# Kernel tuning notes

Hardware: AMD Instinct MI355X
Metric: run time of the kernel (lower is better)

The kernel has to match this reference:

```python
import jax, jax.numpy as jnp
import numpy as np

B, T, C, H, DI = 4, 1024, 1024, 16, 128
TAU = 1.0
LAMBDA_CONF = 0.1
SYS2_THR = 1.0


def _ln(x, w, b):
    mu = x.mean(-1, keepdims=True)
    var = x.var(-1, keepdims=True)
    return (x - mu) * jax.lax.rsqrt(var + 1e-5) * w + b


def setup_inputs() -> dict:
    key = jax.random.key(0)
    ks = jax.random.split(key, 16)
    s = lambda i, shape: jax.random.normal(ks[i], shape, jnp.float32) * 0.02
    return {
        "h": jax.random.normal(ks[0], (B, T, C), jnp.float32),
        "ln_w": jnp.ones((C,), jnp.float32), "ln_b": jnp.zeros((C,), jnp.float32),
        "w_q": s(1, (C, C)), "w_k": s(2, (C, C)), "w_v": s(3, (C, C)),
        "w_o": s(4, (C, C)), "b_o": jnp.zeros((C,), jnp.float32),
        "U": s(5, (C, DI)), "V": s(6, (DI, C)),
        "gamma_w": s(7, (C, 1)), "gamma_b": jnp.zeros((1,), jnp.float32),
        "mass_w": s(8, (C, 1)), "mass_b": jnp.zeros((1,), jnp.float32),
        "eps_w": s(9, (C, 1)), "eps_b": jnp.zeros((1,), jnp.float32),
        "lg_w1": s(10, (C, 4 * C)), "lg_b1": jnp.zeros((4 * C,), jnp.float32),
        "lg_w2": s(11, (4 * C, C)), "lg_b2": jnp.zeros((C,), jnp.float32),
        "mlp_w1": s(12, (C, 4 * C)), "mlp_b1": jnp.zeros((4 * C,), jnp.float32),
        "mlp_w2": s(13, (4 * C, C)), "mlp_b2": jnp.zeros((C,), jnp.float32),
    }


def reference(h, ln_w, ln_b, w_q, w_k, w_v, w_o, b_o, U, V,
              gamma_w, gamma_b, mass_w, mass_b, eps_w, eps_b,
              lg_w1, lg_b1, lg_w2, lg_b2, mlp_w1, mlp_b1, mlp_w2, mlp_b2):
    hd = C // H
    h_norm = _ln(h, ln_w, ln_b)

    # ---- HamiltonianAttention (conservative force field) ----
    q = (h_norm @ w_q).reshape(B, T, H, hd).transpose(0, 2, 1, 3)  # [B,H,T,hd]
    k = (h_norm @ w_k).reshape(B, T, H, hd).transpose(0, 2, 1, 3)
    v = (h_norm @ w_v).reshape(B, T, H, hd).transpose(0, 2, 1, 3)
    scores = jnp.einsum('bhqd,bhkd->bhqk', q, k) / (hd ** 0.5) / TAU
    attn = jax.nn.softmax(scores, axis=-1)
    force = jnp.einsum('bhqk,bhkd->bhqd', attn, v).transpose(0, 2, 1, 3).reshape(B, T, C)
    f_attn = force @ w_o + b_o

    # ---- total force, low-rank projection ----
    f_total = f_attn - LAMBDA_CONF * h_norm
    f_proj = f_total @ U                               # [B,T,DI]

    # ---- FSI (force stability index) ----
    h_mag = jnp.linalg.norm(h_norm, axis=-1)           # [B,T]
    f_mag = jnp.linalg.norm(f_proj, axis=-1)
    fsi = h_mag / (2.0 * f_mag + 1e-6)

    # ---- CognitiveGearbox: per-token mass / timestep ----
    mass = 1.0 + jax.nn.softplus(h @ mass_w + mass_b)  # [B,T,1], mass >= 1
    eps = jax.nn.sigmoid(h @ eps_w + eps_b)            # [B,T,1], eps in (0,1)
    gamma = jax.nn.sigmoid(h_norm @ gamma_w + gamma_b) # [B,T,1] damping gate

    # ---- fused AGI momentum recurrence: m_t = gamma_t*m_{t-1} + (eps_t/mass_t)*f_t ----
    def step(m, inps):
        f_t, g_t, e_t, ms_t = inps                     # [B,DI],[B,1],[B,1],[B,1]
        m = g_t * m + (e_t / ms_t) * f_t
        return m, m

    xs = (f_proj.transpose(1, 0, 2), gamma.transpose(1, 0, 2),
          eps.transpose(1, 0, 2), mass.transpose(1, 0, 2))
    m0 = jnp.zeros((B, DI), h.dtype)
    _, m_seq = jax.lax.scan(step, m0, xs)              # [T,B,DI]
    m_new = m_seq.transpose(1, 0, 2)                   # [B,T,DI]

    # ---- position update + system-2 correction + MLP ----
    velocity = m_new @ V                               # [B,T,C]
    h_new = h + eps * velocity
    hn2 = _ln(h_new, ln_w, ln_b)
    sys2 = jax.nn.gelu(hn2 @ lg_w1 + lg_b1, approximate=False) @ lg_w2 + lg_b2
    gate = jax.nn.sigmoid(mass - SYS2_THR)
    h_final = h_new + gate * sys2
    hn3 = _ln(h_final, ln_w, ln_b)
    h_final = h_final + (jax.nn.gelu(hn3 @ mlp_w1 + mlp_b1, approximate=False) @ mlp_w2 + mlp_b2)
    return (h_final, m_new, fsi)
```

## Files before the change

### kernel.cpp

```cpp
#include <hip/hip_runtime.h>
#include <hip/hip_bf16.h>
#include <math.h>

typedef __attribute__((ext_vector_type(8))) short bf16x8;
typedef __attribute__((ext_vector_type(4))) float f32x4;

#define DEVI __device__ __forceinline__

constexpr int B_ = 4, T_ = 1024, C_ = 1024, H_ = 16, HD_ = 64, DI_ = 128;
constexpr int NTOK = B_ * T_;
constexpr int C4 = 4 * C_;
constexpr int C3 = 3 * C_;
constexpr float LAMBDA_CONF = 0.1f;

DEVI short f2bf(float f) {
  unsigned u = __builtin_bit_cast(unsigned, f);
  u += 0x7fffu + ((u >> 16) & 1u);
  return (short)(u >> 16);
}
DEVI unsigned pk2(float a, float b) {
  return (unsigned)(unsigned short)f2bf(a) | ((unsigned)(unsigned short)f2bf(b) << 16);
}
DEVI float sigm(float x) { return 1.f / (1.f + __expf(-x)); }
DEVI float geluf(float x) { return 0.5f * x * (1.f + erff(x * 0.70710678118654752440f)); }

DEVI void gload16(const void* g, void* l) {
  __builtin_amdgcn_global_load_lds((const __attribute__((address_space(1))) unsigned*)g,
                                   (__attribute__((address_space(3))) unsigned*)l, 16, 0, 0);
}

template <int EPI>
DEVI void epi_store(void* Outp, const float* bias, const float* resid, const float* tokv,
                    int row, int col, int N, float v) {
  size_t idx = (size_t)row * N + col;
  if (EPI == 0) {
    ((float*)Outp)[idx] = v;
  } else if (EPI == 1) {
    ((short*)Outp)[idx] = f2bf(v);
  } else if (EPI == 2) {
    ((short*)Outp)[idx] = f2bf(v + bias[col] - LAMBDA_CONF * resid[idx]);
  } else if (EPI == 3) {
    ((float*)Outp)[idx] = resid[idx] + tokv[row] * v;
  } else if (EPI == 4) {
    float x = v + bias[col];
    ((short*)Outp)[idx] = f2bf(geluf(x));
  } else if (EPI == 5) {
    float x = v + bias[col];
    float g = sigm(tokv[row] - 1.f);
    ((float*)Outp)[idx] = resid[idx] + g * x;
  } else if (EPI == 6) {
    ((float*)Outp)[idx] = resid[idx] + v + bias[col];
  }
}

__global__ __launch_bounds__(256) void transpose_cvt(const float* __restrict__ W,
                                                     short* __restrict__ Wt, int K, int N) {
  __shared__ float s[32][33];
  int n0 = blockIdx.x * 32, k0 = blockIdx.y * 32;
  int tx = threadIdx.x & 31, ty = threadIdx.x >> 5;
#pragma unroll
  for (int i = 0; i < 4; i++)
    s[ty + i * 8][tx] = W[(size_t)(k0 + ty + i * 8) * N + n0 + tx];
  __syncthreads();
#pragma unroll
  for (int i = 0; i < 4; i++)
    Wt[(size_t)(n0 + ty + i * 8) * K + k0 + tx] = f2bf(s[tx][ty + i * 8]);
}

__global__ __launch_bounds__(256) void transpose_v(const short* __restrict__ QKV,
                                                   short* __restrict__ VT) {
  __shared__ short s[32][33];
  int bh = blockIdx.z;
  int b = bh >> 4, h = bh & 15;
  int t0 = blockIdx.x * 32, d0 = blockIdx.y * 32;
  int tx = threadIdx.x & 31, ty = threadIdx.x >> 5;
#pragma unroll
  for (int i = 0; i < 4; i++)
    s[ty + i * 8][tx] =
        QKV[(size_t)(b * T_ + t0 + ty + i * 8) * C3 + 2 * C_ + h * 64 + d0 + tx];
  __syncthreads();
#pragma unroll
  for (int i = 0; i < 4; i++)
    VT[((size_t)bh * 64 + d0 + ty + i * 8) * T_ + t0 + tx] = s[tx][ty + i * 8];
}

DEVI float blk_red(float v, volatile float* sm) {
  int lane = threadIdx.x & 63, wv = threadIdx.x >> 6;
#pragma unroll
  for (int o = 32; o; o >>= 1) v += __shfl_down(v, o);
  __syncthreads();
  if (lane == 0) sm[wv] = v;
  __syncthreads();
  return sm[0] + sm[1] + sm[2] + sm[3];
}

template <int FULL, int WF32>
__global__ __launch_bounds__(256) void ln_kernel(
    const float* __restrict__ X, const float* __restrict__ lnw, const float* __restrict__ lnb,
    float* __restrict__ Out, short* __restrict__ OutBf,
    const float* __restrict__ gw, const float* __restrict__ gb,
    const float* __restrict__ mw, const float* __restrict__ mb,
    const float* __restrict__ ew, const float* __restrict__ eb,
    float* __restrict__ gammaA, float* __restrict__ epsA, float* __restrict__ massA,
    float* __restrict__ coefA, float* __restrict__ hmagA) {
  __shared__ float sm[4];
  int tok = blockIdx.x;
  const float* x = X + (size_t)tok * C_;
  int t4 = threadIdx.x * 4;
  float4 xv = *(const float4*)&x[t4];
  float s = xv.x + xv.y + xv.z + xv.w;
  float ss = xv.x * xv.x + xv.y * xv.y + xv.z * xv.z + xv.w * xv.w;
  s = blk_red(s, sm);
  ss = blk_red(ss, sm);
  float mu = s * (1.f / C_);
  float var = ss * (1.f / C_) - mu * mu;
  float rs = rsqrtf(var + 1e-5f);
  float4 wv = *(const float4*)&lnw[t4];
  float4 bv = *(const float4*)&lnb[t4];
  float4 hn;
  hn.x = (xv.x - mu) * rs * wv.x + bv.x;
  hn.y = (xv.y - mu) * rs * wv.y + bv.y;
  hn.z = (xv.z - mu) * rs * wv.z + bv.z;
  hn.w = (xv.w - mu) * rs * wv.w + bv.w;
  if (WF32) *(float4*)&Out[(size_t)tok * C_ + t4] = hn;
  short4 ob;
  ob.x = f2bf(hn.x); ob.y = f2bf(hn.y); ob.z = f2bf(hn.z); ob.w = f2bf(hn.w);
  *(short4*)&OutBf[(size_t)tok * C_ + t4] = ob;
  if (FULL) {
    float4 gwv = *(const float4*)&gw[t4];
    float4 mwv = *(const float4*)&mw[t4];
    float4 ewv = *(const float4*)&ew[t4];
    float gd = hn.x * gwv.x + hn.y * gwv.y + hn.z * gwv.z + hn.w * gwv.w;
    float md = xv.x * mwv.x + xv.y * mwv.y + xv.z * mwv.z + xv.w * mwv.w;
    float ed = xv.x * ewv.x + xv.y * ewv.y + xv.z * ewv.z + xv.w * ewv.w;
    float h2 = hn.x * hn.x + hn.y * hn.y + hn.z * hn.z + hn.w * hn.w;
    gd = blk_red(gd, sm);
    md = blk_red(md, sm);
    ed = blk_red(ed, sm);
    h2 = blk_red(h2, sm);
    if (threadIdx.x == 0) {
      float g = sigm(gd + gb[0]);
      float xm = md + mb[0];
      float sp = (xm > 20.f) ? xm : log1pf(expf(xm));
      float msv = 1.f + sp;
      float epv = sigm(ed + eb[0]);
      gammaA[tok] = g;
      massA[tok] = msv;
      epsA[tok] = epv;
      coefA[tok] = epv / msv;
      hmagA[tok] = sqrtf(h2);
    }
  }
}

template <int EPI, int NB>
__global__ __launch_bounds__(256, 3) void gemmS(
    const short* __restrict__ A, const short* __restrict__ Bt, void* __restrict__ Outp,
    const float* __restrict__ bias, const float* __restrict__ resid,
    const float* __restrict__ tokv, int M, int N, int K) {
  constexpr int NT = NB / 64;
  constexpr int NFR = NB / 32;
  __shared__ short As[128][32];
  __shared__ short Bs[NB][32];
  int tid = threadIdx.x, lane = tid & 63, w = tid >> 6;
  int wr = w >> 1, wc = w & 1;
  int fr = lane & 15, fg = lane >> 4;
  int xm = (fr >> 1) & 3;
  int nM = M >> 7;
  int cpx = gridDim.x >> 3;
  int bid = (blockIdx.x & 7) * cpx + (blockIdx.x >> 3);
  int bm = (bid % nM) << 7;
  int bn = (bid / nM) * NB;
  f32x4 acc[4][NFR] = {};

  int jsw = (lane & 3) ^ ((lane >> 3) & 3);
  const short* gA = A + (size_t)(bm + w * 32 + (lane >> 2)) * K + (jsw << 3);
  const short* gB;
  if constexpr (NB == 128)
    gB = Bt + (size_t)(bn + w * 32 + (lane >> 2)) * K + (jsw << 3);
  else
    gB = Bt + (size_t)(bn + w * 16 + (lane >> 2)) * K + (jsw << 3);

  for (int kt = 0; kt < K; kt += 32) {
    gload16(gA + kt, &As[w * 32][0]);
    gload16(gA + (size_t)16 * K + kt, &As[w * 32 + 16][0]);
    if constexpr (NB == 128) {
      gload16(gB + kt, &Bs[w * 32][0]);
      gload16(gB + (size_t)16 * K + kt, &Bs[w * 32 + 16][0]);
    } else {
      gload16(gB + kt, &Bs[w * 16][0]);
    }
    __syncthreads();
    bf16x8 af[4], bv[NFR];
#pragma unroll
    for (int i = 0; i < 4; i++)
      af[i] = *(const bf16x8*)&As[wr * 64 + i * 16 + fr][(fg ^ xm) << 3];
#pragma unroll
    for (int j = 0; j < NFR; j++)
      bv[j] = *(const bf16x8*)&Bs[wc * (NB / 2) + j * 16 + fr][(fg ^ xm) << 3];
#pragma unroll
    for (int mi = 0; mi < 4; mi++)
#pragma unroll
      for (int ni = 0; ni < NFR; ni++)
        acc[mi][ni] = __builtin_amdgcn_mfma_f32_16x16x32_bf16(af[mi], bv[ni], acc[mi][ni], 0, 0, 0);
    __syncthreads();
  }

#pragma unroll
  for (int mi = 0; mi < 4; mi++) {
    int row0 = bm + wr * 64 + mi * 16 + fg * 4;
#pragma unroll
    for (int ni = 0; ni < NFR; ni++) {
      int col = bn + wc * (NB / 2) + ni * 16 + fr;
#pragma unroll
      for (int r = 0; r < 4; r++)
        epi_store<EPI>(Outp, bias, resid, tokv, row0 + r, col, N, acc[mi][ni][r]);
    }
  }
}

template <int EPI, int MT, int NT>
__global__ __launch_bounds__(512) void gemmP(
    const short* __restrict__ A, const short* __restrict__ Bt, void* __restrict__ Outp,
    const float* __restrict__ bias, const float* __restrict__ resid,
    const float* __restrict__ tokv, int M, int N, int K) {
  constexpr int BM = 4 * MT * 16;
  constexpr int BN = 2 * NT * 16;
  constexpr int CA = BM / 64;
  constexpr int CB = BN / 64;
  constexpr int LPT = CA + CB;
  __shared__ short As[3][BM][64];
  __shared__ short Bs[3][BN][64];
  int tid = threadIdx.x, lane = tid & 63, w = tid >> 6;
  int wr = w >> 1, wc = w & 1;
  int fr = lane & 15, fg = lane >> 4;
  int nMt = M / BM;
  int cpx = gridDim.x >> 3;
  int gbid = (blockIdx.x & 7) * cpx + (blockIdx.x >> 3);
  int chunk = gbid >> 5;
  int wi = gbid & 31;
  int nCM = nMt >> 2;
  int bm = ((chunk % nCM) * 4 + (wi & 3)) * BM;
  int bn = ((chunk / nCM) * 8 + (wi >> 2)) * BN;
  f32x4 acc[MT][NT] = {};

  int jsw = (lane & 7) ^ ((lane >> 3) & 7);
  const short* gA = A + (size_t)(bm + w * 8 + (lane >> 3)) * K + (jsw << 3);
  const short* gB = Bt + (size_t)(bn + w * 8 + (lane >> 3)) * K + (jsw << 3);

  auto stage = [&](int buf, int kt) {
#pragma unroll
    for (int c = 0; c < CA; c++)
      gload16(gA + (size_t)(c * 64) * K + kt, &As[buf][c * 64 + w * 8][0]);
#pragma unroll
    for (int c = 0; c < CB; c++)
      gload16(gB + (size_t)(c * 64) * K + kt, &Bs[buf][c * 64 + w * 8][0]);
  };

  int nt = K >> 6;
  stage(0, 0);
  if (nt > 1) stage(1, 64);
  for (int t = 0; t < nt; t++) {
    if (t + 1 < nt) {
      if constexpr (LPT == 6) asm volatile("s_waitcnt vmcnt(6)" ::: "memory");
      else asm volatile("s_waitcnt vmcnt(4)" ::: "memory");
    } else {
      asm volatile("s_waitcnt vmcnt(0)" ::: "memory");
    }
    __builtin_amdgcn_s_barrier();
    __builtin_amdgcn_sched_barrier(0);
    int nb = t + 2;
    if (nb < nt) stage(nb % 3, nb << 6);
    int cb = t % 3;
    short(*Ac)[64] = As[cb];
    short(*Bc)[64] = Bs[cb];
    bf16x8 af[MT], bv[NT / 2];
#pragma unroll
    for (int kh = 0; kh < 2; kh++) {
#pragma unroll
      for (int i = 0; i < MT; i++) {
        int row = wr * (MT * 16) + i * 16 + fr;
        af[i] = *(const bf16x8*)&Ac[row][((((kh << 2) | fg)) ^ (fr & 7)) << 3];
      }
#pragma unroll
      for (int nh = 0; nh < 2; nh++) {
#pragma unroll
        for (int j = 0; j < NT / 2; j++) {
          int row = wc * (NT * 16) + nh * (NT / 2) * 16 + j * 16 + fr;
          bv[j] = *(const bf16x8*)&Bc[row][((((kh << 2) | fg)) ^ (fr & 7)) << 3];
        }
#pragma unroll
        for (int i = 0; i < MT; i++)
#pragma unroll
          for (int j = 0; j < NT / 2; j++)
            acc[i][nh * (NT / 2) + j] = __builtin_amdgcn_mfma_f32_16x16x32_bf16(
                af[i], bv[j], acc[i][nh * (NT / 2) + j], 0, 0, 0);
      }
    }
  }

#pragma unroll
  for (int mi = 0; mi < MT; mi++) {
    int row0 = bm + wr * (MT * 16) + mi * 16 + fg * 4;
#pragma unroll
    for (int ni = 0; ni < NT; ni++) {
      int col = bn + wc * (NT * 16) + ni * 16 + fr;
#pragma unroll
      for (int r = 0; r < 4; r++)
        epi_store<EPI>(Outp, bias, resid, tokv, row0 + r, col, N, acc[mi][ni][r]);
    }
  }
}

template <int EPI>
__global__ __launch_bounds__(256) void gemm128(
    const short* __restrict__ A, const short* __restrict__ Bt, void* __restrict__ Outp,
    const float* __restrict__ bias, const float* __restrict__ resid,
    const float* __restrict__ tokv, int M, int N, int K) {
  __shared__ short As[3][128][32];
  __shared__ short Bs[3][128][32];
  int tid = threadIdx.x, lane = tid & 63, w = tid >> 6;
  int wr = w >> 1, wc = w & 1;
  int fr = lane & 15, fg = lane >> 4;
  int xm = (fr >> 1) & 3;
  int nM = M >> 7;
  int cpx = gridDim.x >> 3;
  int bid = (blockIdx.x & 7) * cpx + (blockIdx.x >> 3);
  int bm = (bid % nM) << 7;
  int bn = (bid / nM) << 7;
  f32x4 acc[4][4] = {};

  int jsw = (lane & 3) ^ ((lane >> 3) & 3);
  const short* gA = A + (size_t)(bm + w * 32 + (lane >> 2)) * K + (jsw << 3);
  const short* gB = Bt + (size_t)(bn + w * 32 + (lane >> 2)) * K + (jsw << 3);

  auto stage = [&](int buf, int kt) {
#pragma unroll
    for (int g = 0; g < 2; g++) {
      gload16(gA + (size_t)(g * 16) * K + kt, &As[buf][w * 32 + g * 16][0]);
      gload16(gB + (size_t)(g * 16) * K + kt, &Bs[buf][w * 32 + g * 16][0]);
    }
  };

  int nt = K >> 5;
  stage(0, 0);
  if (nt > 1) stage(1, 32);
  for (int t = 0; t < nt; t++) {
    if (t + 1 < nt) asm volatile("s_waitcnt vmcnt(4)" ::: "memory");
    else asm volatile("s_waitcnt vmcnt(0)" ::: "memory");
    __builtin_amdgcn_s_barrier();
    __builtin_amdgcn_sched_barrier(0);
    int nb = t + 2;
    if (nb < nt) stage(nb % 3, nb << 5);
    int cb = t % 3;
    bf16x8 af[4], bfv[4];
#pragma unroll
    for (int i = 0; i < 4; i++)
      af[i] = *(const bf16x8*)&As[cb][wr * 64 + i * 16 + fr][(fg ^ xm) << 3];
#pragma unroll
    for (int i = 0; i < 4; i++)
      bfv[i] = *(const bf16x8*)&Bs[cb][wc * 64 + i * 16 + fr][(fg ^ xm) << 3];
#pragma unroll
    for (int mi = 0; mi < 4; mi++)
#pragma unroll
      for (int ni = 0; ni < 4; ni++)
        acc[mi][ni] = __builtin_amdgcn_mfma_f32_16x16x32_bf16(af[mi], bfv[ni], acc[mi][ni], 0, 0, 0);
  }

#pragma unroll
  for (int mi = 0; mi < 4; mi++) {
    int row0 = bm + wr * 64 + mi * 16 + fg * 4;
#pragma unroll
    for (int ni = 0; ni < 4; ni++) {
      int col = bn + wc * 64 + ni * 16 + fr;
#pragma unroll
      for (int r = 0; r < 4; r++)
        epi_store<EPI>(Outp, bias, resid, tokv, row0 + r, col, N, acc[mi][ni][r]);
    }
  }
}

__global__ __launch_bounds__(256) void attn_kernel(const short* __restrict__ QKV,
                                                   const short* __restrict__ VT,
                                                   short* __restrict__ Fout) {
  __shared__ short Ks[2][64][64];
  __shared__ short Vts[2][64][64];
  __shared__ short Ps[4][16][72];
  int bh = blockIdx.y;
  int b = bh >> 4, h = bh & 15;
  int qt0 = blockIdx.x * 64;
  int tid = threadIdx.x, lane = tid & 63, w = tid >> 6;
  int fr = lane & 15, fg = lane >> 4;

  size_t base = ((size_t)b * T_) * C3 + h * 64;
  const short* Qp = QKV + base;
  const short* Kp = QKV + base + C_;
  const short* Vtp = VT + (size_t)bh * 64 * T_;
  int qrow = qt0 + w * 16 + fr;
  bf16x8 qf0 = *(const bf16x8*)&Qp[(size_t)qrow * C3 + fg * 8];
  bf16x8 qf1 = *(const bf16x8*)&Qp[(size_t)qrow * C3 + 32 + fg * 8];

  f32x4 oacc[4] = {};
  float m_run = -1e30f, l_run = 0.f;

  int jsw = (lane & 7) ^ ((lane >> 3) & 7);
  int sr8 = w * 8;
  int rsub = lane >> 3;

  auto stage = [&](int buf, int kt) {
#pragma unroll
    for (int c = 0; c < 2; c++) {
      int row = c * 32 + sr8 + rsub;
      gload16(Kp + (size_t)(kt + row) * C3 + jsw * 8, &Ks[buf][c * 32 + sr8][0]);
      gload16(Vtp + (size_t)row * T_ + kt + jsw * 8, &Vts[buf][c * 32 + sr8][0]);
    }
  };

  stage(0, 0);
  for (int t = 0; t < T_ / 64; t++) {
    if (t + 1 < T_ / 64) {
      stage((t + 1) & 1, (t + 1) * 64);
      asm volatile("s_waitcnt vmcnt(4)" ::: "memory");
    } else {
      asm volatile("s_waitcnt vmcnt(0)" ::: "memory");
    }
    __builtin_amdgcn_s_barrier();
    __builtin_amdgcn_sched_barrier(0);
    int cb = t & 1;

    f32x4 sacc[4];
#pragma unroll
    for (int kb = 0; kb < 4; kb++) {
      bf16x8 k0 = *(const bf16x8*)&Ks[cb][kb * 16 + fr][(fg ^ (fr & 7)) << 3];
      bf16x8 k1 = *(const bf16x8*)&Ks[cb][kb * 16 + fr][((4 | fg) ^ (fr & 7)) << 3];
      f32x4 z = {};
      z = __builtin_amdgcn_mfma_f32_16x16x32_bf16(k0, qf0, z, 0, 0, 0);
      z = __builtin_amdgcn_mfma_f32_16x16x32_bf16(k1, qf1, z, 0, 0, 0);
      sacc[kb] = z;
    }
    float mt = -1e30f;
#pragma unroll
    for (int kb = 0; kb < 4; kb++)
#pragma unroll
      for (int r = 0; r < 4; r++) {
        sacc[kb][r] *= 0.125f;
        mt = fmaxf(mt, sacc[kb][r]);
      }
    mt = fmaxf(mt, __shfl_xor(mt, 16));
    mt = fmaxf(mt, __shfl_xor(mt, 32));
    float m_new = fmaxf(m_run, mt);
    float alpha = __expf(m_run - m_new);
    float psum = 0.f;
    float pv[16];
#pragma unroll
    for (int kb = 0; kb < 4; kb++)
#pragma unroll
      for (int r = 0; r < 4; r++) {
        float p = __expf(sacc[kb][r] - m_new);
        pv[kb * 4 + r] = p;
        psum += p;
      }
    psum += __shfl_xor(psum, 16);
    psum += __shfl_xor(psum, 32);
    l_run = l_run * alpha + psum;
    m_run = m_new;

#pragma unroll
    for (int kb = 0; kb < 4; kb++) {
      uint2 pp;
      pp.x = pk2(pv[kb * 4 + 0], pv[kb * 4 + 1]);
      pp.y = pk2(pv[kb * 4 + 2], pv[kb * 4 + 3]);
      *(uint2*)&Ps[w][fr][kb * 16 + fg * 4] = pp;
    }
    float ar[4];
#pragma unroll
    for (int r = 0; r < 4; r++) ar[r] = __shfl(alpha, fg * 4 + r);
#pragma unroll
    for (int ni = 0; ni < 4; ni++)
#pragma unroll
      for (int r = 0; r < 4; r++) oacc[ni][r] *= ar[r];

    asm volatile("s_waitcnt lgkmcnt(0)" ::: "memory");
    __builtin_amdgcn_sched_barrier(0);
    bf16x8 pa0 = *(const bf16x8*)&Ps[w][fr][fg * 8];
    bf16x8 pa1 = *(const bf16x8*)&Ps[w][fr][32 + fg * 8];
#pragma unroll
    for (int ni = 0; ni < 4; ni++) {
      bf16x8 v0 = *(const bf16x8*)&Vts[cb][ni * 16 + fr][(fg ^ (fr & 7)) << 3];
      bf16x8 v1 = *(const bf16x8*)&Vts[cb][ni * 16 + fr][((4 | fg) ^ (fr & 7)) << 3];
      oacc[ni] = __builtin_amdgcn_mfma_f32_16x16x32_bf16(pa0, v0, oacc[ni], 0, 0, 0);
      oacc[ni] = __builtin_amdgcn_mfma_f32_16x16x32_bf16(pa1, v1, oacc[ni], 0, 0, 0);
    }
    __builtin_amdgcn_s_barrier();
  }

  float lr4[4];
#pragma unroll
  for (int r = 0; r < 4; r++) lr4[r] = __shfl(l_run, fg * 4 + r);
#pragma unroll
  for (int ni = 0; ni < 4; ni++)
#pragma unroll
    for (int r = 0; r < 4; r++) {
      int tok = b * T_ + qt0 + w * 16 + fg * 4 + r;
      Fout[(size_t)tok * C_ + h * 64 + ni * 16 + fr] = f2bf(oacc[ni][r] / lr4[r]);
    }
}

__global__ __launch_bounds__(128) void scan_kernel(const float* __restrict__ f_proj,
                                                   const float* __restrict__ gam,
                                                   const float* __restrict__ coef,
                                                   float* __restrict__ m_out,
                                                   short* __restrict__ m_bf) {
  int b = blockIdx.x;
  int d = threadIdx.x;
  const float* fp = f_proj + (size_t)b * T_ * DI_ + d;
  const float* g = gam + (size_t)b * T_;
  const float* c = coef + (size_t)b * T_;
  float* mo = m_out + (size_t)b * T_ * DI_ + d;
  short* mb = m_bf + (size_t)b * T_ * DI_ + d;
  float m = 0.f;
  for (int t = 0; t < T_; t += 8) {
    float fv[8], gv[8], cv[8];
#pragma unroll
    for (int i = 0; i < 8; i++) {
      fv[i] = fp[(size_t)(t + i) * DI_];
      gv[i] = g[t + i];
      cv[i] = c[t + i];
    }
#pragma unroll
    for (int i = 0; i < 8; i++) {
      m = gv[i] * m + cv[i] * fv[i];
      mo[(size_t)(t + i) * DI_] = m;
      mb[(size_t)(t + i) * DI_] = f2bf(m);
    }
  }
}

__global__ __launch_bounds__(256) void fsi_kernel(const float* __restrict__ f_proj,
                                                  const float* __restrict__ hmag,
                                                  float* __restrict__ fsi_out) {
  int tok = blockIdx.x * 4 + (threadIdx.x >> 6);
  int l = threadIdx.x & 63;
  float2 v = *(const float2*)&f_proj[(size_t)tok * DI_ + l * 2];
  float s = v.x * v.x + v.y * v.y;
#pragma unroll
  for (int o = 32; o; o >>= 1) s += __shfl_down(s, o);
  if (l == 0) fsi_out[tok] = hmag[tok] / (2.f * sqrtf(s) + 1e-6f);
}

extern "C" void kernel_launch(void* const* d_in, const int* in_sizes, int n_in,
                              void* d_out, int out_size, void* d_ws, size_t ws_size,
                              hipStream_t stream) {
  (void)in_sizes; (void)n_in; (void)out_size; (void)ws_size;
  const float* h = (const float*)d_in[0];
  const float* ln_w = (const float*)d_in[1];
  const float* ln_b = (const float*)d_in[2];
  const float* w_q = (const float*)d_in[3];
  const float* w_k = (const float*)d_in[4];
  const float* w_v = (const float*)d_in[5];
  const float* w_o = (const float*)d_in[6];
  const float* b_o = (const float*)d_in[7];
  const float* U = (const float*)d_in[8];
  const float* V = (const float*)d_in[9];
  const float* gamma_w = (const float*)d_in[10];
  const float* gamma_b = (const float*)d_in[11];
  const float* mass_w = (const float*)d_in[12];
  const float* mass_b = (const float*)d_in[13];
  const float* eps_w = (const float*)d_in[14];
  const float* eps_b = (const float*)d_in[15];
  const float* lg_w1 = (const float*)d_in[16];
  const float* lg_b1 = (const float*)d_in[17];
  const float* lg_w2 = (const float*)d_in[18];
  const float* lg_b2 = (const float*)d_in[19];
  const float* mlp_w1 = (const float*)d_in[20];
  const float* mlp_b1 = (const float*)d_in[21];
  const float* mlp_w2 = (const float*)d_in[22];
  const float* mlp_b2 = (const float*)d_in[23];

  float* out_h = (float*)d_out;
  float* out_m = out_h + (size_t)NTOK * C_;
  float* out_fsi = out_m + (size_t)NTOK * DI_;

  char* wsb = (char*)d_ws;
  size_t off = 0;
  auto al = [&](size_t bytes) {
    void* p = wsb + off;
    off += (bytes + 255) & ~(size_t)255;
    return p;
  };
  short* wqkvt = (short*)al((size_t)C3 * C_ * 2);
  short* wot = (short*)al((size_t)C_ * C_ * 2);
  short* ut = (short*)al((size_t)DI_ * C_ * 2);
  short* vt = (short*)al((size_t)C_ * DI_ * 2);
  short* lg1t = (short*)al((size_t)C4 * C_ * 2);
  short* lg2t = (short*)al((size_t)C_ * C4 * 2);
  short* mlp1t = (short*)al((size_t)C4 * C_ * 2);
  short* mlp2t = (short*)al((size_t)C_ * C4 * 2);
  float* h_norm = (float*)al((size_t)NTOK * C_ * 4);
  short* hn_bf = (short*)al((size_t)NTOK * C_ * 2);
  short* qkv_bf = (short*)al((size_t)NTOK * C3 * 2);
  short* tmp_bf = (short*)al((size_t)NTOK * C_ * 2);
  float* f_proj = (float*)al((size_t)NTOK * DI_ * 4);
  short* act = (short*)al((size_t)NTOK * C4 * 2);
  float* h_pre = (float*)al((size_t)NTOK * C_ * 4);
  short* vtrans = (short*)al((size_t)B_ * H_ * 64 * T_ * 2);
  float* gammaA = (float*)al((size_t)NTOK * 4);
  float* epsA = (float*)al((size_t)NTOK * 4);
  float* massA = (float*)al((size_t)NTOK * 4);
  float* coefA = (float*)al((size_t)NTOK * 4);
  float* hmagA = (float*)al((size_t)NTOK * 4);
  short* ftot_bf = hn_bf;
  short* m_bf = act;
  float* h_new = (float*)qkv_bf;

  dim3 blk(256);
  dim3 blk512(512);
  transpose_cvt<<<dim3(C_ / 32, C_ / 32), blk, 0, stream>>>(w_q, wqkvt, C_, C_);
  transpose_cvt<<<dim3(C_ / 32, C_ / 32), blk, 0, stream>>>(w_k, wqkvt + (size_t)C_ * C_, C_, C_);
  transpose_cvt<<<dim3(C_ / 32, C_ / 32), blk, 0, stream>>>(w_v, wqkvt + (size_t)2 * C_ * C_, C_, C_);
  transpose_cvt<<<dim3(C_ / 32, C_ / 32), blk, 0, stream>>>(w_o, wot, C_, C_);
  transpose_cvt<<<dim3(DI_ / 32, C_ / 32), blk, 0, stream>>>(U, ut, C_, DI_);
  transpose_cvt<<<dim3(C_ / 32, DI_ / 32), blk, 0, stream>>>(V, vt, DI_, C_);
  transpose_cvt<<<dim3(C4 / 32, C_ / 32), blk, 0, stream>>>(lg_w1, lg1t, C_, C4);
  transpose_cvt<<<dim3(C_ / 32, C4 / 32), blk, 0, stream>>>(lg_w2, lg2t, C4, C_);
  transpose_cvt<<<dim3(C4 / 32, C_ / 32), blk, 0, stream>>>(mlp_w1, mlp1t, C_, C4);
  transpose_cvt<<<dim3(C_ / 32, C4 / 32), blk, 0, stream>>>(mlp_w2, mlp2t, C4, C_);

  ln_kernel<1, 1><<<NTOK, blk, 0, stream>>>(h, ln_w, ln_b, h_norm, hn_bf, gamma_w, gamma_b,
                                            mass_w, mass_b, eps_w, eps_b, gammaA, epsA, massA,
                                            coefA, hmagA);
  gemmS<1, 128><<<(NTOK / 128) * (C3 / 128), blk, 0, stream>>>(hn_bf, wqkvt, qkv_bf, nullptr,
                                                               nullptr, nullptr, NTOK, C3, C_);
  transpose_v<<<dim3(T_ / 32, 2, B_ * H_), blk, 0, stream>>>(qkv_bf, vtrans);
  attn_kernel<<<dim3(T_ / 64, B_ * H_), blk, 0, stream>>>(qkv_bf, vtrans, tmp_bf);
  gemmP<2, 2, 4><<<(NTOK / 128) * (C_ / 128), blk512, 0, stream>>>(tmp_bf, wot, ftot_bf, b_o,
                                                                   h_norm, nullptr, NTOK, C_, C_);
  gemm128<0><<<(NTOK / 128) * (DI_ / 128), blk, 0, stream>>>(ftot_bf, ut, f_proj, nullptr,
                                                             nullptr, nullptr, NTOK, DI_, C_);
  fsi_kernel<<<NTOK / 4, blk, 0, stream>>>(f_proj, hmagA, out_fsi);
  scan_kernel<<<B_, dim3(DI_), 0, stream>>>(f_proj, gammaA, coefA, out_m, m_bf);
  gemmP<3, 2, 4><<<(NTOK / 128) * (C_ / 128), blk512, 0, stream>>>(m_bf, vt, h_new, nullptr, h,
                                                                   epsA, NTOK, C_, DI_);
  ln_kernel<0, 0><<<NTOK, blk, 0, stream>>>(h_new, ln_w, ln_b, nullptr, tmp_bf, nullptr, nullptr,
                                            nullptr, nullptr, nullptr, nullptr, nullptr, nullptr,
                                            nullptr, nullptr, nullptr);
  gemmS<4, 128><<<(NTOK / 128) * (C4 / 128), blk, 0, stream>>>(tmp_bf, lg1t, act, lg_b1,
                                                               nullptr, nullptr, NTOK, C4, C_);
  gemmS<5, 64><<<(NTOK / 128) * (C_ / 64), blk, 0, stream>>>(act, lg2t, h_pre, lg_b2,
                                                             h_new, massA, NTOK, C_, C4);
  ln_kernel<0, 0><<<NTOK, blk, 0, stream>>>(h_pre, ln_w, ln_b, nullptr, tmp_bf, nullptr, nullptr,
                                            nullptr, nullptr, nullptr, nullptr, nullptr, nullptr,
                                            nullptr, nullptr, nullptr);
  gemmS<4, 128><<<(NTOK / 128) * (C4 / 128), blk, 0, stream>>>(tmp_bf, mlp1t, act, mlp_b1,
                                                               nullptr, nullptr, NTOK, C4, C_);
  gemmS<6, 64><<<(NTOK / 128) * (C_ / 64), blk, 0, stream>>>(act, mlp2t, out_h, mlp_b2,
                                                             h_pre, nullptr, NTOK, C_, C4);
}
```

Before: 503.2 us.

## Replace pipelined gemmP with gemmS, add N-fast tile ordering and sched barriers

Measured after the change: 523.8 us. +4.1%, slower.

```diff
diff --git a/kernel.cpp b/kernel.cpp
--- a/kernel.cpp
+++ b/kernel.cpp
@@ -153,12 +153,11 @@
   }
 }
 
-template <int EPI, int NB>
+template <int EPI, int NB, int BNFAST>
 __global__ __launch_bounds__(256, 3) void gemmS(
     const short* __restrict__ A, const short* __restrict__ Bt, void* __restrict__ Outp,
     const float* __restrict__ bias, const float* __restrict__ resid,
     const float* __restrict__ tokv, int M, int N, int K) {
-  constexpr int NT = NB / 64;
   constexpr int NFR = NB / 32;
   __shared__ short As[128][32];
   __shared__ short Bs[NB][32];
@@ -166,11 +165,18 @@
   int wr = w >> 1, wc = w & 1;
   int fr = lane & 15, fg = lane >> 4;
   int xm = (fr >> 1) & 3;
-  int nM = M >> 7;
   int cpx = gridDim.x >> 3;
   int bid = (blockIdx.x & 7) * cpx + (blockIdx.x >> 3);
-  int bm = (bid % nM) << 7;
-  int bn = (bid / nM) * NB;
+  int bm, bn;
+  if constexpr (BNFAST) {
+    int nN = N / NB;
+    bn = (bid % nN) * NB;
+    bm = (bid / nN) << 7;
+  } else {
+    int nM = M >> 7;
+    bm = (bid % nM) << 7;
+    bn = (bid / nM) * NB;
+  }
   f32x4 acc[4][NFR] = {};
 
   int jsw = (lane & 3) ^ ((lane >> 3) & 3);
@@ -212,99 +218,6 @@
 #pragma unroll
     for (int ni = 0; ni < NFR; ni++) {
       int col = bn + wc * (NB / 2) + ni * 16 + fr;
-#pragma unroll
-      for (int r = 0; r < 4; r++)
-        epi_store<EPI>(Outp, bias, resid, tokv, row0 + r, col, N, acc[mi][ni][r]);
-    }
-  }
-}
-
-template <int EPI, int MT, int NT>
-__global__ __launch_bounds__(512) void gemmP(
-    const short* __restrict__ A, const short* __restrict__ Bt, void* __restrict__ Outp,
-    const float* __restrict__ bias, const float* __restrict__ resid,
-    const float* __restrict__ tokv, int M, int N, int K) {
-  constexpr int BM = 4 * MT * 16;
-  constexpr int BN = 2 * NT * 16;
-  constexpr int CA = BM / 64;
-  constexpr int CB = BN / 64;
-  constexpr int LPT = CA + CB;
-  __shared__ short As[3][BM][64];
-  __shared__ short Bs[3][BN][64];
-  int tid = threadIdx.x, lane = tid & 63, w = tid >> 6;
-  int wr = w >> 1, wc = w & 1;
-  int fr = lane & 15, fg = lane >> 4;
-  int nMt = M / BM;
-  int cpx = gridDim.x >> 3;
-  int gbid = (blockIdx.x & 7) * cpx + (blockIdx.x >> 3);
-  int chunk = gbid >> 5;
-  int wi = gbid & 31;
-  int nCM = nMt >> 2;
-  int bm = ((chunk % nCM) * 4 + (wi & 3)) * BM;
-  int bn = ((chunk / nCM) * 8 + (wi >> 2)) * BN;
-  f32x4 acc[MT][NT] = {};
-
-  int jsw = (lane & 7) ^ ((lane >> 3) & 7);
-  const short* gA = A + (size_t)(bm + w * 8 + (lane >> 3)) * K + (jsw << 3);
-  const short* gB = Bt + (size_t)(bn + w * 8 + (lane >> 3)) * K + (jsw << 3);
-
-  auto stage = [&](int buf, int kt) {
-#pragma unroll
-    for (int c = 0; c < CA; c++)
-      gload16(gA + (size_t)(c * 64) * K + kt, &As[buf][c * 64 + w * 8][0]);
-#pragma unroll
-    for (int c = 0; c < CB; c++)
-      gload16(gB + (size_t)(c * 64) * K + kt, &Bs[buf][c * 64 + w * 8][0]);
-  };
-
-  int nt = K >> 6;
-  stage(0, 0);
-  if (nt > 1) stage(1, 64);
-  for (int t = 0; t < nt; t++) {
-    if (t + 1 < nt) {
-      if constexpr (LPT == 6) asm volatile("s_waitcnt vmcnt(6)" ::: "memory");
-      else asm volatile("s_waitcnt vmcnt(4)" ::: "memory");
-    } else {
-      asm volatile("s_waitcnt vmcnt(0)" ::: "memory");
-    }
-    __builtin_amdgcn_s_barrier();
-    __builtin_amdgcn_sched_barrier(0);
-    int nb = t + 2;
-    if (nb < nt) stage(nb % 3, nb << 6);
-    int cb = t % 3;
-    short(*Ac)[64] = As[cb];
-    short(*Bc)[64] = Bs[cb];
-    bf16x8 af[MT], bv[NT / 2];
-#pragma unroll
-    for (int kh = 0; kh < 2; kh++) {
-#pragma unroll
-      for (int i = 0; i < MT; i++) {
-        int row = wr * (MT * 16) + i * 16 + fr;
-        af[i] = *(const bf16x8*)&Ac[row][((((kh << 2) | fg)) ^ (fr & 7)) << 3];
-      }
-#pragma unroll
-      for (int nh = 0; nh < 2; nh++) {
-#pragma unroll
-        for (int j = 0; j < NT / 2; j++) {
-          int row = wc * (NT * 16) + nh * (NT / 2) * 16 + j * 16 + fr;
-          bv[j] = *(const bf16x8*)&Bc[row][((((kh << 2) | fg)) ^ (fr & 7)) << 3];
-        }
-#pragma unroll
-        for (int i = 0; i < MT; i++)
-#pragma unroll
-          for (int j = 0; j < NT / 2; j++)
-            acc[i][nh * (NT / 2) + j] = __builtin_amdgcn_mfma_f32_16x16x32_bf16(
-                af[i], bv[j], acc[i][nh * (NT / 2) + j], 0, 0, 0);
-      }
-    }
-  }
-
-#pragma unroll
-  for (int mi = 0; mi < MT; mi++) {
-    int row0 = bm + wr * (MT * 16) + mi * 16 + fg * 4;
-#pragma unroll
-    for (int ni = 0; ni < NT; ni++) {
-      int col = bn + wc * (NT * 16) + ni * 16 + fr;
 #pragma unroll
       for (int r = 0; r < 4; r++)
         epi_store<EPI>(Outp, bias, resid, tokv, row0 + r, col, N, acc[mi][ni][r]);
@@ -365,6 +278,8 @@
 #pragma unroll
       for (int ni = 0; ni < 4; ni++)
         acc[mi][ni] = __builtin_amdgcn_mfma_f32_16x16x32_bf16(af[mi], bfv[ni], acc[mi][ni], 0, 0, 0);
+    __builtin_amdgcn_sched_barrier(0);
+    __builtin_amdgcn_s_barrier();
   }
 
 #pragma unroll
@@ -491,6 +406,7 @@
       oacc[ni] = __builtin_amdgcn_mfma_f32_16x16x32_bf16(pa0, v0, oacc[ni], 0, 0, 0);
       oacc[ni] = __builtin_amdgcn_mfma_f32_16x16x32_bf16(pa1, v1, oacc[ni], 0, 0, 0);
     }
+    __builtin_amdgcn_sched_barrier(0);
     __builtin_amdgcn_s_barrier();
   }
 
@@ -614,7 +530,6 @@
   float* h_new = (float*)qkv_bf;
 
   dim3 blk(256);
-  dim3 blk512(512);
   transpose_cvt<<<dim3(C_ / 32, C_ / 32), blk, 0, stream>>>(w_q, wqkvt, C_, C_);
   transpose_cvt<<<dim3(C_ / 32, C_ / 32), blk, 0, stream>>>(w_k, wqkvt + (size_t)C_ * C_, C_, C_);
   transpose_cvt<<<dim3(C_ / 32, C_ / 32), blk, 0, stream>>>(w_v, wqkvt + (size_t)2 * C_ * C_, C_, C_);
@@ -629,30 +544,30 @@
   ln_kernel<1, 1><<<NTOK, blk, 0, stream>>>(h, ln_w, ln_b, h_norm, hn_bf, gamma_w, gamma_b,
                                             mass_w, mass_b, eps_w, eps_b, gammaA, epsA, massA,
                                             coefA, hmagA);
-  gemmS<1, 128><<<(NTOK / 128) * (C3 / 128), blk, 0, stream>>>(hn_bf, wqkvt, qkv_bf, nullptr,
-                                                               nullptr, nullptr, NTOK, C3, C_);
+  gemmS<1, 128, 0><<<(NTOK / 128) * (C3 / 128), blk, 0, stream>>>(hn_bf, wqkvt, qkv_bf, nullptr,
+                                                                  nullptr, nullptr, NTOK, C3, C_);
   transpose_v<<<dim3(T_ / 32, 2, B_ * H_), blk, 0, stream>>>(qkv_bf, vtrans);
   attn_kernel<<<dim3(T_ / 64, B_ * H_), blk, 0, stream>>>(qkv_bf, vtrans, tmp_bf);
-  gemmP<2, 2, 4><<<(NTOK / 128) * (C_ / 128), blk512, 0, stream>>>(tmp_bf, wot, ftot_bf, b_o,
-                                                                   h_norm, nullptr, NTOK, C_, C_);
+  gemmS<2, 64, 1><<<(NTOK / 128) * (C_ / 64), blk, 0, stream>>>(tmp_bf, wot, ftot_bf, b_o,
+                                                                h_norm, nullptr, NTOK, C_, C_);
   gemm128<0><<<(NTOK / 128) * (DI_ / 128), blk, 0, stream>>>(ftot_bf, ut, f_proj, nullptr,
                                                              nullptr, nullptr, NTOK, DI_, C_);
   fsi_kernel<<<NTOK / 4, blk, 0, stream>>>(f_proj, hmagA, out_fsi);
   scan_kernel<<<B_, dim3(DI_), 0, stream>>>(f_proj, gammaA, coefA, out_m, m_bf);
-  gemmP<3, 2, 4><<<(NTOK / 128) * (C_ / 128), blk512, 0, stream>>>(m_bf, vt, h_new, nullptr, h,
-                                                                   epsA, NTOK, C_, DI_);
+  gemmS<3, 64, 0><<<(NTOK / 128) * (C_ / 64), blk, 0, stream>>>(m_bf, vt, h_new, nullptr, h,
+                                                                epsA, NTOK, C_, DI_);
   ln_kernel<0, 0><<<NTOK, blk, 0, stream>>>(h_new, ln_w, ln_b, nullptr, tmp_bf, nullptr, nullptr,
                                             nullptr, nullptr, nullptr, nullptr, nullptr, nullptr,
                                             nullptr, nullptr, nullptr);
-  gemmS<4, 128><<<(NTOK / 128) * (C4 / 128), blk, 0, stream>>>(tmp_bf, lg1t, act, lg_b1,
-                                                               nullptr, nullptr, NTOK, C4, C_);
-  gemmS<5, 64><<<(NTOK / 128) * (C_ / 64), blk, 0, stream>>>(act, lg2t, h_pre, lg_b2,
-                                                             h_new, massA, NTOK, C_, C4);
+  gemmS<4, 128, 0><<<(NTOK / 128) * (C4 / 128), blk, 0, stream>>>(tmp_bf, lg1t, act, lg_b1,
+                                                                  nullptr, nullptr, NTOK, C4, C_);
+  gemmS<5, 64, 1><<<(NTOK / 128) * (C_ / 64), blk, 0, stream>>>(act, lg2t, h_pre, lg_b2,
+                                                                h_new, massA, NTOK, C_, C4);
   ln_kernel<0, 0><<<NTOK, blk, 0, stream>>>(h_pre, ln_w, ln_b, nullptr, tmp_bf, nullptr, nullptr,
                                             nullptr, nullptr, nullptr, nullptr, nullptr, nullptr,
                                             nullptr, nullptr, nullptr);
-  gemmS<4, 128><<<(NTOK / 128) * (C4 / 128), blk, 0, stream>>>(tmp_bf, mlp1t, act, mlp_b1,
-                                                               nullptr, nullptr, NTOK, C4, C_);
-  gemmS<6, 64><<<(NTOK / 128) * (C_ / 64), blk, 0, stream>>>(act, mlp2t, out_h, mlp_b2,
-                                                             h_pre, nullptr, NTOK, C_, C4);
-}
+  gemmS<4, 128, 0><<<(NTOK / 128) * (C4 / 128), blk, 0, stream>>>(tmp_bf, mlp1t, act, mlp_b1,
+                                                                  nullptr, nullptr, NTOK, C4, C_);
+  gemmS<6, 64, 1><<<(NTOK / 128) * (C_ / 64), blk, 0, stream>>>(act, mlp2t, out_h, mlp_b2,
+                                                                h_pre, nullptr, NTOK, C_, C4);
+}
```
